# Kernel optimization log

Measured on AMD Instinct MI355X. Metric: run time of the kernel, lower is better.

The kernel has to match this reference:

```python
import jax, jax.numpy as jnp
import numpy as np

B, S, D = 4, 2048, 1024
O = 1024
E = 8
K = 2

def setup_inputs() -> dict:
    key = jax.random.key(0)
    k1, k2, k3, k4, k5 = jax.random.split(key, 5)
    scale = 1.0 / np.sqrt(D)
    x = jax.random.normal(k1, (B, S, D), dtype=jnp.float32)
    # expert linear layers stacked: weight [E, D, O], bias [E, O]
    We = jax.random.uniform(k2, (E, D, O), dtype=jnp.float32, minval=-scale, maxval=scale)
    be = jax.random.uniform(k3, (E, O), dtype=jnp.float32, minval=-scale, maxval=scale)
    # gate linear: weight [D, E], bias [E]
    Wg = jax.random.uniform(k4, (D, E), dtype=jnp.float32, minval=-scale, maxval=scale)
    bg = jax.random.uniform(k5, (E,), dtype=jnp.float32, minval=-scale, maxval=scale)
    return {"x": x, "We": We, "be": be, "Wg": Wg, "bg": bg}

def reference(x, We, be, Wg, bg):
    b, s, d = x.shape
    x_flat = x.reshape(-1, d)                                   # [N, D]
    gates = jax.nn.softmax(x_flat @ Wg + bg, axis=-1)           # [N, E]
    topk_gates, topk_idx = jax.lax.top_k(gates, K)              # [N, K]
    topk_gates = topk_gates / jnp.sum(topk_gates, axis=1, keepdims=True)
    # dense all-expert compute (faithful to original naive MoE)
    expert_out = jnp.einsum('nd,edo->neo', x_flat, We) + be     # [N, E, O]
    # gather top-k expert outputs per token
    selected = jnp.take_along_axis(expert_out, topk_idx[:, :, None], axis=1)  # [N, K, O]
    out = jnp.sum(selected * topk_gates[:, :, None], axis=1)    # [N, O]
    return out.reshape(b, s, -1)
```

## Files before the change

kernel.cpp:

```cpp
#include <hip/hip_runtime.h>

#define N_TOK 8192
#define DDIM 1024
#define ODIM 1024
#define NEXP 8

typedef __attribute__((ext_vector_type(8))) short bf16x8;
typedef __attribute__((ext_vector_type(4))) float f32x4;

__device__ __forceinline__ unsigned int f2bf(float f) {
    unsigned int u = __float_as_uint(f);
    return (u + 0x7fffu + ((u >> 16) & 1u)) >> 16;
}
__device__ __forceinline__ float bflo(unsigned int u) { return __uint_as_float(u << 16); }
__device__ __forceinline__ float bfhi(unsigned int u) { return __uint_as_float(u & 0xffff0000u); }

__device__ __forceinline__ void async_copy16(const unsigned short* g, unsigned short* l) {
    __builtin_amdgcn_global_load_lds(
        (const __attribute__((address_space(1))) unsigned int*)g,
        (__attribute__((address_space(3))) unsigned int*)l, 16, 0, 0);
}

__global__ __launch_bounds__(256) void gate_kernel(const float* __restrict__ x,
                                                   const float* __restrict__ Wg,
                                                   const float* __restrict__ bg,
                                                   int* __restrict__ ea, int* __restrict__ eb,
                                                   float* __restrict__ ga, float* __restrict__ gb,
                                                   unsigned short* __restrict__ xbf,
                                                   int* __restrict__ counts) {
    if (blockIdx.x == 0) counts[threadIdx.x] = 0;
    const int wave = threadIdx.x >> 6, lane = threadIdx.x & 63;
    const int t = blockIdx.x * 4 + wave;
    const float* xr = x + (size_t)t * DDIM;

    float4 v[4];
#pragma unroll
    for (int c = 0; c < 4; ++c) v[c] = *(const float4*)&xr[c * 256 + lane * 4];

    unsigned short* xo = xbf + (size_t)t * DDIM;
#pragma unroll
    for (int c = 0; c < 4; ++c) {
        uint2 w;
        w.x = f2bf(v[c].x) | (f2bf(v[c].y) << 16);
        w.y = f2bf(v[c].z) | (f2bf(v[c].w) << 16);
        *(uint2*)&xo[c * 256 + lane * 4] = w;
    }

    float acc[8] = {0, 0, 0, 0, 0, 0, 0, 0};
#pragma unroll
    for (int c = 0; c < 4; ++c) {
        const int dbase = c * 256 + lane * 4;
#pragma unroll
        for (int j = 0; j < 4; ++j) {
            float xv = ((const float*)&v[c])[j];
            const float4* w = (const float4*)(Wg + (size_t)(dbase + j) * 8);
            float4 w0 = w[0], w1 = w[1];
            acc[0] += xv * w0.x; acc[1] += xv * w0.y; acc[2] += xv * w0.z; acc[3] += xv * w0.w;
            acc[4] += xv * w1.x; acc[5] += xv * w1.y; acc[6] += xv * w1.z; acc[7] += xv * w1.w;
        }
    }
#pragma unroll
    for (int off = 32; off > 0; off >>= 1) {
#pragma unroll
        for (int j = 0; j < 8; ++j) acc[j] += __shfl_xor(acc[j], off, 64);
    }
    if (lane == 0) {
        float s[8];
#pragma unroll
        for (int e = 0; e < 8; ++e) s[e] = acc[e] + bg[e];
        int a = 0;
#pragma unroll
        for (int e = 1; e < 8; ++e) if (s[e] > s[a]) a = e;
        int b = (a == 0) ? 1 : 0;
#pragma unroll
        for (int e = 0; e < 8; ++e) if (e != a && e != b && s[e] > s[b]) b = e;
        float g0 = 1.0f / (1.0f + __expf(s[b] - s[a]));
        ea[t] = a; eb[t] = b; ga[t] = g0; gb[t] = 1.0f - g0;
    }
}

__global__ __launch_bounds__(256) void transpose_kernel(const float* __restrict__ We,
                                                        unsigned short* __restrict__ WeT) {
    __shared__ float tile[64][65];
    const int lin = blockIdx.x;
    const int e = lin >> 8, rem = lin & 255;
    const int d0 = (rem >> 4) * 64, o0 = (rem & 15) * 64;
    const int tid = threadIdx.x;
#pragma unroll
    for (int p = 0; p < 4; ++p) {
        int idx = p * 256 + tid;
        int row = idx >> 4, c = idx & 15;
        float4 v = *(const float4*)&We[(((size_t)e * 1024 + d0 + row) << 10) + o0 + (c << 2)];
        tile[row][c * 4 + 0] = v.x; tile[row][c * 4 + 1] = v.y;
        tile[row][c * 4 + 2] = v.z; tile[row][c * 4 + 3] = v.w;
    }
    __syncthreads();
#pragma unroll
    for (int p = 0; p < 2; ++p) {
        int idx = p * 256 + tid;
        int orow = idx >> 3, c8 = idx & 7;
        unsigned int u[8];
#pragma unroll
        for (int j = 0; j < 8; ++j) u[j] = f2bf(tile[c8 * 8 + j][orow]);
        uint4 q;
        q.x = u[0] | (u[1] << 16); q.y = u[2] | (u[3] << 16);
        q.z = u[4] | (u[5] << 16); q.w = u[6] | (u[7] << 16);
        *(uint4*)&WeT[(((size_t)e * 1024 + o0 + orow) << 10) + d0 + (c8 << 3)] = q;
    }
}

__global__ __launch_bounds__(64) void scatter_kernel(const int* __restrict__ ea,
                                                     const int* __restrict__ eb,
                                                     int* __restrict__ counts,
                                                     int* __restrict__ btok,
                                                     int* __restrict__ slotA,
                                                     int* __restrict__ slotB) {
    const int t = blockIdx.x * 64 + threadIdx.x;
    const int lane = threadIdx.x & 63;
#pragma unroll
    for (int pass = 0; pass < 2; ++pass) {
        const int e = (pass == 0) ? ea[t] : eb[t];
        int* slot = (pass == 0) ? slotA : slotB;
#pragma unroll
        for (int ex = 0; ex < NEXP; ++ex) {
            unsigned long long mask = __ballot(e == ex);
            if (mask) {
                int leader = __ffsll((long long)mask) - 1;
                int base = 0;
                if (lane == leader) base = atomicAdd(&counts[ex * 32], __popcll(mask));
                base = __shfl(base, leader, 64);
                if (e == ex) {
                    int pos = base + __popcll(mask & ((1ull << lane) - 1ull));
                    btok[ex * N_TOK + pos] = t;
                    slot[t] = ex * N_TOK + pos;
                }
            }
        }
    }
}

__global__ __launch_bounds__(256, 2) void moe_gemm(const unsigned short* __restrict__ xbf,
                                                   const unsigned short* __restrict__ WeT,
                                                   const float* __restrict__ be,
                                                   const int* __restrict__ counts,
                                                   const int* __restrict__ btok,
                                                   unsigned short* __restrict__ ybuf) {
    const int id = blockIdx.x;
    const int e = id & 7;
    const int n0 = ((id >> 3) & 7) * 128;
    const int r0 = (id >> 6) * 160;
    const int cnt = counts[e * 32];
    if (r0 >= cnt) return;

    __shared__ unsigned short smem[36864];
    __shared__ int s_tok[160];

    const int tid = threadIdx.x;
    if (tid < 160) {
        int r = r0 + tid;
        int rc = (r < cnt) ? r : (cnt - 1);
        s_tok[tid] = btok[e * N_TOK + rc];
    }
    const int w = tid >> 6, lane = tid & 63;
    __syncthreads();

    const int rsub = lane >> 3;
    const int colo = ((lane & 7) ^ rsub) * 8;
    unsigned int a_off[5], b_off[4];
#pragma unroll
    for (int p = 0; p < 5; ++p) {
        int row = p * 32 + w * 8 + rsub;
        a_off[p] = ((unsigned)s_tok[row] << 10) + colo;
    }
#pragma unroll
    for (int p = 0; p < 4; ++p) {
        int row = p * 32 + w * 8 + rsub;
        b_off[p] = ((unsigned)(e * 1024 + n0 + row) << 10) + colo;
    }
    const int ldsrow = w * 8;

    const int wm = (w >> 1) * 80, wn = (w & 1) * 64;
    const int quad = lane >> 4, rA = lane & 15;
    const int sw = rA & 7;
    const int cs0 = (quad ^ sw) * 8;
    const int cs1 = ((4 + quad) ^ sw) * 8;

    f32x4 acc[5][4];
#pragma unroll
    for (int mi = 0; mi < 5; ++mi)
#pragma unroll
        for (int ni = 0; ni < 4; ++ni) acc[mi][ni] = (f32x4){0.f, 0.f, 0.f, 0.f};

#pragma unroll
    for (int p = 0; p < 5; ++p)
        async_copy16(xbf + a_off[p], &smem[(p * 32 + ldsrow) * 64]);
#pragma unroll
    for (int p = 0; p < 4; ++p)
        async_copy16(WeT + b_off[p], &smem[20480 + (p * 32 + ldsrow) * 64]);
#pragma unroll
    for (int p = 0; p < 5; ++p)
        async_copy16(xbf + a_off[p] + 64, &smem[10240 + (p * 32 + ldsrow) * 64]);
#pragma unroll
    for (int p = 0; p < 4; ++p)
        async_copy16(WeT + b_off[p] + 64, &smem[28672 + (p * 32 + ldsrow) * 64]);
    asm volatile("s_waitcnt vmcnt(9)" ::: "memory");
    __builtin_amdgcn_s_barrier();
    __builtin_amdgcn_sched_barrier(0);

    bf16x8 a0[5], b0[4];
#pragma unroll
    for (int i = 0; i < 5; ++i) a0[i] = *(bf16x8*)&smem[(wm + i * 16 + rA) * 64 + cs0];
#pragma unroll
    for (int i = 0; i < 4; ++i) b0[i] = *(bf16x8*)&smem[20480 + (wn + i * 16 + rA) * 64 + cs0];

    for (int t = 0; t < 16; ++t) {
        const int cur = t & 1;
        unsigned short* sAc = smem + cur * 10240;
        unsigned short* sBc = smem + 20480 + cur * 8192;
        unsigned short* sAn = smem + (cur ^ 1) * 10240;
        unsigned short* sBn = smem + 20480 + (cur ^ 1) * 8192;

        bf16x8 a1[5], b1[4];
#pragma unroll
        for (int i = 0; i < 5; ++i) a1[i] = *(bf16x8*)&sAc[(wm + i * 16 + rA) * 64 + cs1];
#pragma unroll
        for (int i = 0; i < 4; ++i) b1[i] = *(bf16x8*)&sBc[(wn + i * 16 + rA) * 64 + cs1];
        __builtin_amdgcn_s_setprio(1);
#pragma unroll
        for (int mi = 0; mi < 5; ++mi)
#pragma unroll
            for (int ni = 0; ni < 4; ++ni)
                acc[mi][ni] = __builtin_amdgcn_mfma_f32_16x16x32_bf16(b0[ni], a0[mi], acc[mi][ni], 0, 0, 0);
        __builtin_amdgcn_s_setprio(0);

        asm volatile("s_waitcnt lgkmcnt(0)" ::: "memory");
        __builtin_amdgcn_sched_barrier(0);
        __builtin_amdgcn_s_barrier();
        __builtin_amdgcn_sched_barrier(0);

        if (t < 14) {
            const int ko = (t + 2) * 64;
#pragma unroll
            for (int p = 0; p < 5; ++p)
                async_copy16(xbf + a_off[p] + ko, &sAc[(p * 32 + ldsrow) * 64]);
#pragma unroll
            for (int p = 0; p < 4; ++p)
                async_copy16(WeT + b_off[p] + ko, &sBc[(p * 32 + ldsrow) * 64]);
        }
        if (t < 15) {
            if (t < 14) {
                asm volatile("s_waitcnt vmcnt(9)" ::: "memory");
            } else {
                asm volatile("s_waitcnt vmcnt(0)" ::: "memory");
            }
            __builtin_amdgcn_sched_barrier(0);
            __builtin_amdgcn_s_barrier();
            __builtin_amdgcn_sched_barrier(0);
#pragma unroll
            for (int i = 0; i < 5; ++i) a0[i] = *(bf16x8*)&sAn[(wm + i * 16 + rA) * 64 + cs0];
#pragma unroll
            for (int i = 0; i < 4; ++i) b0[i] = *(bf16x8*)&sBn[(wn + i * 16 + rA) * 64 + cs0];
        }

        __builtin_amdgcn_s_setprio(1);
#pragma unroll
        for (int mi = 0; mi < 5; ++mi)
#pragma unroll
            for (int ni = 0; ni < 4; ++ni)
                acc[mi][ni] = __builtin_amdgcn_mfma_f32_16x16x32_bf16(b1[ni], a1[mi], acc[mi][ni], 0, 0, 0);
        __builtin_amdgcn_s_setprio(0);
    }

    float4 bv[4];
#pragma unroll
    for (int ni = 0; ni < 4; ++ni)
        bv[ni] = *(const float4*)&be[(e << 10) + n0 + wn + ni * 16 + quad * 4];
#pragma unroll
    for (int mi = 0; mi < 5; ++mi) {
        const int lrow = wm + mi * 16 + rA;
        if (r0 + lrow < cnt) {
            unsigned short* yrow =
                ybuf + (((size_t)(e * N_TOK + r0 + lrow)) << 10) + n0 + wn + quad * 4;
#pragma unroll
            for (int ni = 0; ni < 4; ++ni) {
                uint2 pk;
                pk.x = f2bf(acc[mi][ni][0] + bv[ni].x) | (f2bf(acc[mi][ni][1] + bv[ni].y) << 16);
                pk.y = f2bf(acc[mi][ni][2] + bv[ni].z) | (f2bf(acc[mi][ni][3] + bv[ni].w) << 16);
                *(uint2*)&yrow[ni * 16] = pk;
            }
        }
    }
}

__global__ __launch_bounds__(256) void combine_kernel(const unsigned short* __restrict__ ybuf,
                                                      const int* __restrict__ slotA,
                                                      const int* __restrict__ slotB,
                                                      const float* __restrict__ ga,
                                                      const float* __restrict__ gb,
                                                      float* __restrict__ out) {
    const int wave = threadIdx.x >> 6, lane = threadIdx.x & 63;
    const int t = blockIdx.x * 4 + wave;
    const unsigned short* ra = ybuf + ((size_t)slotA[t] << 10);
    const unsigned short* rb = ybuf + ((size_t)slotB[t] << 10);
    const float a = ga[t], b = gb[t];
    float* orow = out + ((size_t)t << 10);
#pragma unroll
    for (int i = 0; i < 2; ++i) {
        int c = i * 512 + lane * 8;
        uint4 ua = *(const uint4*)&ra[c];
        uint4 ub = *(const uint4*)&rb[c];
        float4 o0, o1;
        o0.x = a * bflo(ua.x) + b * bflo(ub.x);
        o0.y = a * bfhi(ua.x) + b * bfhi(ub.x);
        o0.z = a * bflo(ua.y) + b * bflo(ub.y);
        o0.w = a * bfhi(ua.y) + b * bfhi(ub.y);
        o1.x = a * bflo(ua.z) + b * bflo(ub.z);
        o1.y = a * bfhi(ua.z) + b * bfhi(ub.z);
        o1.z = a * bflo(ua.w) + b * bflo(ub.w);
        o1.w = a * bfhi(ua.w) + b * bfhi(ub.w);
        *(float4*)&orow[c] = o0;
        *(float4*)&orow[c + 4] = o1;
    }
}

extern "C" void kernel_launch(void* const* d_in, const int* in_sizes, int n_in,
                              void* d_out, int out_size, void* d_ws, size_t ws_size,
                              hipStream_t stream) {
    const float* x  = (const float*)d_in[0];
    const float* We = (const float*)d_in[1];
    const float* be = (const float*)d_in[2];
    const float* Wg = (const float*)d_in[3];
    const float* bg = (const float*)d_in[4];
    float* out = (float*)d_out;

    char* ws = (char*)d_ws;
    size_t off = 0;
    int* counts = (int*)(ws + off); off += 8 * 32 * 4;
    int* btok   = (int*)(ws + off); off += NEXP * N_TOK * 4;
    int* slotA  = (int*)(ws + off); off += N_TOK * 4;
    int* slotB  = (int*)(ws + off); off += N_TOK * 4;
    int* ea = (int*)(ws + off); off += N_TOK * 4;
    int* eb = (int*)(ws + off); off += N_TOK * 4;
    float* ga = (float*)(ws + off); off += N_TOK * 4;
    float* gb = (float*)(ws + off); off += N_TOK * 4;
    unsigned short* WeT  = (unsigned short*)(ws + off); off += (size_t)NEXP * DDIM * ODIM * 2;
    unsigned short* xbf  = (unsigned short*)(ws + off); off += (size_t)N_TOK * DDIM * 2;
    unsigned short* ybuf = (unsigned short*)(ws + off); off += (size_t)NEXP * N_TOK * ODIM * 2;

    gate_kernel<<<dim3(2048), 256, 0, stream>>>(x, Wg, bg, ea, eb, ga, gb, xbf, counts);
    transpose_kernel<<<dim3(2048), 256, 0, stream>>>(We, WeT);
    scatter_kernel<<<dim3(N_TOK / 64), 64, 0, stream>>>(ea, eb, counts, btok, slotA, slotB);
    moe_gemm<<<dim3(64 * 8 * 8), 256, 0, stream>>>(xbf, WeT, be, counts, btok, ybuf);
    combine_kernel<<<dim3(N_TOK / 4), 256, 0, stream>>>(ybuf, slotA, slotB, ga, gb, out);
}
```

Measured before the change: 208.6 us.

## Fuse gate and transpose kernels, replace combine pass with atomic accumulation in GEMM epilogue

The gate and weight-transpose kernels merge into one prep kernel, which also zero-initialises the output. The separate combine kernel and the bf16 ybuf intermediate are removed. The GEMM epilogue now scales each row by its gate weight and float-atomically adds it directly into the output row of its token. This removes the write and re-read of the large expert-output buffer and one launch, at the cost of scalar float atomics and non-deterministic summation order.

After: 392.3 us. 88.0% more time.

```diff
diff --git a/kernel.cpp b/kernel.cpp
--- a/kernel.cpp
+++ b/kernel.cpp
@@ -12,8 +12,6 @@
     unsigned int u = __float_as_uint(f);
     return (u + 0x7fffu + ((u >> 16) & 1u)) >> 16;
 }
-__device__ __forceinline__ float bflo(unsigned int u) { return __uint_as_float(u << 16); }
-__device__ __forceinline__ float bfhi(unsigned int u) { return __uint_as_float(u & 0xffff0000u); }
 
 __device__ __forceinline__ void async_copy16(const unsigned short* g, unsigned short* l) {
     __builtin_amdgcn_global_load_lds(
@@ -21,106 +19,114 @@
         (__attribute__((address_space(3))) unsigned int*)l, 16, 0, 0);
 }
 
-__global__ __launch_bounds__(256) void gate_kernel(const float* __restrict__ x,
+__global__ __launch_bounds__(256) void prep_kernel(const float* __restrict__ x,
                                                    const float* __restrict__ Wg,
                                                    const float* __restrict__ bg,
+                                                   const float* __restrict__ We,
                                                    int* __restrict__ ea, int* __restrict__ eb,
                                                    float* __restrict__ ga, float* __restrict__ gb,
                                                    unsigned short* __restrict__ xbf,
-                                                   int* __restrict__ counts) {
-    if (blockIdx.x == 0) counts[threadIdx.x] = 0;
-    const int wave = threadIdx.x >> 6, lane = threadIdx.x & 63;
-    const int t = blockIdx.x * 4 + wave;
-    const float* xr = x + (size_t)t * DDIM;
-
-    float4 v[4];
-#pragma unroll
-    for (int c = 0; c < 4; ++c) v[c] = *(const float4*)&xr[c * 256 + lane * 4];
-
-    unsigned short* xo = xbf + (size_t)t * DDIM;
-#pragma unroll
-    for (int c = 0; c < 4; ++c) {
-        uint2 w;
-        w.x = f2bf(v[c].x) | (f2bf(v[c].y) << 16);
-        w.y = f2bf(v[c].z) | (f2bf(v[c].w) << 16);
-        *(uint2*)&xo[c * 256 + lane * 4] = w;
-    }
-
-    float acc[8] = {0, 0, 0, 0, 0, 0, 0, 0};
-#pragma unroll
-    for (int c = 0; c < 4; ++c) {
-        const int dbase = c * 256 + lane * 4;
-#pragma unroll
-        for (int j = 0; j < 4; ++j) {
-            float xv = ((const float*)&v[c])[j];
-            const float4* w = (const float4*)(Wg + (size_t)(dbase + j) * 8);
-            float4 w0 = w[0], w1 = w[1];
-            acc[0] += xv * w0.x; acc[1] += xv * w0.y; acc[2] += xv * w0.z; acc[3] += xv * w0.w;
-            acc[4] += xv * w1.x; acc[5] += xv * w1.y; acc[6] += xv * w1.z; acc[7] += xv * w1.w;
-        }
-    }
-#pragma unroll
-    for (int off = 32; off > 0; off >>= 1) {
-#pragma unroll
-        for (int j = 0; j < 8; ++j) acc[j] += __shfl_xor(acc[j], off, 64);
-    }
-    if (lane == 0) {
-        float s[8];
-#pragma unroll
-        for (int e = 0; e < 8; ++e) s[e] = acc[e] + bg[e];
-        int a = 0;
-#pragma unroll
-        for (int e = 1; e < 8; ++e) if (s[e] > s[a]) a = e;
-        int b = (a == 0) ? 1 : 0;
-#pragma unroll
-        for (int e = 0; e < 8; ++e) if (e != a && e != b && s[e] > s[b]) b = e;
-        float g0 = 1.0f / (1.0f + __expf(s[b] - s[a]));
-        ea[t] = a; eb[t] = b; ga[t] = g0; gb[t] = 1.0f - g0;
-    }
-}
-
-__global__ __launch_bounds__(256) void transpose_kernel(const float* __restrict__ We,
-                                                        unsigned short* __restrict__ WeT) {
+                                                   unsigned short* __restrict__ WeT,
+                                                   int* __restrict__ counts,
+                                                   float* __restrict__ out) {
     __shared__ float tile[64][65];
-    const int lin = blockIdx.x;
-    const int e = lin >> 8, rem = lin & 255;
-    const int d0 = (rem >> 4) * 64, o0 = (rem & 15) * 64;
-    const int tid = threadIdx.x;
-#pragma unroll
-    for (int p = 0; p < 4; ++p) {
-        int idx = p * 256 + tid;
-        int row = idx >> 4, c = idx & 15;
-        float4 v = *(const float4*)&We[(((size_t)e * 1024 + d0 + row) << 10) + o0 + (c << 2)];
-        tile[row][c * 4 + 0] = v.x; tile[row][c * 4 + 1] = v.y;
-        tile[row][c * 4 + 2] = v.z; tile[row][c * 4 + 3] = v.w;
-    }
-    __syncthreads();
-#pragma unroll
-    for (int p = 0; p < 2; ++p) {
-        int idx = p * 256 + tid;
-        int orow = idx >> 3, c8 = idx & 7;
-        unsigned int u[8];
-#pragma unroll
-        for (int j = 0; j < 8; ++j) u[j] = f2bf(tile[c8 * 8 + j][orow]);
-        uint4 q;
-        q.x = u[0] | (u[1] << 16); q.y = u[2] | (u[3] << 16);
-        q.z = u[4] | (u[5] << 16); q.w = u[6] | (u[7] << 16);
-        *(uint4*)&WeT[(((size_t)e * 1024 + o0 + orow) << 10) + d0 + (c8 << 3)] = q;
+    if (blockIdx.x < 2048) {
+        if (blockIdx.x == 0) counts[threadIdx.x] = 0;
+        const int wave = threadIdx.x >> 6, lane = threadIdx.x & 63;
+        const int t = blockIdx.x * 4 + wave;
+        const float* xr = x + (size_t)t * DDIM;
+
+        float* orow = out + ((size_t)t << 10);
+        const float4 z = {0.f, 0.f, 0.f, 0.f};
+#pragma unroll
+        for (int c = 0; c < 4; ++c) *(float4*)&orow[c * 256 + lane * 4] = z;
+
+        float4 v[4];
+#pragma unroll
+        for (int c = 0; c < 4; ++c) v[c] = *(const float4*)&xr[c * 256 + lane * 4];
+
+        unsigned short* xo = xbf + (size_t)t * DDIM;
+#pragma unroll
+        for (int c = 0; c < 4; ++c) {
+            uint2 w;
+            w.x = f2bf(v[c].x) | (f2bf(v[c].y) << 16);
+            w.y = f2bf(v[c].z) | (f2bf(v[c].w) << 16);
+            *(uint2*)&xo[c * 256 + lane * 4] = w;
+        }
+
+        float acc[8] = {0, 0, 0, 0, 0, 0, 0, 0};
+#pragma unroll
+        for (int c = 0; c < 4; ++c) {
+            const int dbase = c * 256 + lane * 4;
+#pragma unroll
+            for (int j = 0; j < 4; ++j) {
+                float xv = ((const float*)&v[c])[j];
+                const float4* w = (const float4*)(Wg + (size_t)(dbase + j) * 8);
+                float4 w0 = w[0], w1 = w[1];
+                acc[0] += xv * w0.x; acc[1] += xv * w0.y; acc[2] += xv * w0.z; acc[3] += xv * w0.w;
+                acc[4] += xv * w1.x; acc[5] += xv * w1.y; acc[6] += xv * w1.z; acc[7] += xv * w1.w;
+            }
+        }
+#pragma unroll
+        for (int off = 32; off > 0; off >>= 1) {
+#pragma unroll
+            for (int j = 0; j < 8; ++j) acc[j] += __shfl_xor(acc[j], off, 64);
+        }
+        if (lane == 0) {
+            float s[8];
+#pragma unroll
+            for (int e = 0; e < 8; ++e) s[e] = acc[e] + bg[e];
+            int a = 0;
+#pragma unroll
+            for (int e = 1; e < 8; ++e) if (s[e] > s[a]) a = e;
+            int b = (a == 0) ? 1 : 0;
+#pragma unroll
+            for (int e = 0; e < 8; ++e) if (e != a && e != b && s[e] > s[b]) b = e;
+            float g0 = 1.0f / (1.0f + __expf(s[b] - s[a]));
+            ea[t] = a; eb[t] = b; ga[t] = g0; gb[t] = 1.0f - g0;
+        }
+    } else {
+        const int lin = blockIdx.x - 2048;
+        const int e = lin >> 8, rem = lin & 255;
+        const int d0 = (rem >> 4) * 64, o0 = (rem & 15) * 64;
+        const int tid = threadIdx.x;
+#pragma unroll
+        for (int p = 0; p < 4; ++p) {
+            int idx = p * 256 + tid;
+            int row = idx >> 4, c = idx & 15;
+            float4 v = *(const float4*)&We[(((size_t)e * 1024 + d0 + row) << 10) + o0 + (c << 2)];
+            tile[row][c * 4 + 0] = v.x; tile[row][c * 4 + 1] = v.y;
+            tile[row][c * 4 + 2] = v.z; tile[row][c * 4 + 3] = v.w;
+        }
+        __syncthreads();
+#pragma unroll
+        for (int p = 0; p < 2; ++p) {
+            int idx = p * 256 + tid;
+            int orow = idx >> 3, c8 = idx & 7;
+            unsigned int u[8];
+#pragma unroll
+            for (int j = 0; j < 8; ++j) u[j] = f2bf(tile[c8 * 8 + j][orow]);
+            uint4 q;
+            q.x = u[0] | (u[1] << 16); q.y = u[2] | (u[3] << 16);
+            q.z = u[4] | (u[5] << 16); q.w = u[6] | (u[7] << 16);
+            *(uint4*)&WeT[(((size_t)e * 1024 + o0 + orow) << 10) + d0 + (c8 << 3)] = q;
+        }
     }
 }
 
 __global__ __launch_bounds__(64) void scatter_kernel(const int* __restrict__ ea,
                                                      const int* __restrict__ eb,
+                                                     const float* __restrict__ ga,
+                                                     const float* __restrict__ gb,
                                                      int* __restrict__ counts,
                                                      int* __restrict__ btok,
-                                                     int* __restrict__ slotA,
-                                                     int* __restrict__ slotB) {
+                                                     float* __restrict__ wtok) {
     const int t = blockIdx.x * 64 + threadIdx.x;
     const int lane = threadIdx.x & 63;
 #pragma unroll
     for (int pass = 0; pass < 2; ++pass) {
         const int e = (pass == 0) ? ea[t] : eb[t];
-        int* slot = (pass == 0) ? slotA : slotB;
+        const float wg = (pass == 0) ? ga[t] : gb[t];
 #pragma unroll
         for (int ex = 0; ex < NEXP; ++ex) {
             unsigned long long mask = __ballot(e == ex);
@@ -132,7 +138,7 @@
                 if (e == ex) {
                     int pos = base + __popcll(mask & ((1ull << lane) - 1ull));
                     btok[ex * N_TOK + pos] = t;
-                    slot[t] = ex * N_TOK + pos;
+                    wtok[ex * N_TOK + pos] = wg;
                 }
             }
         }
@@ -144,7 +150,8 @@
                                                    const float* __restrict__ be,
                                                    const int* __restrict__ counts,
                                                    const int* __restrict__ btok,
-                                                   unsigned short* __restrict__ ybuf) {
+                                                   const float* __restrict__ wtok,
+                                                   float* __restrict__ out) {
     const int id = blockIdx.x;
     const int e = id & 7;
     const int n0 = ((id >> 3) & 7) * 128;
@@ -279,47 +286,17 @@
     for (int mi = 0; mi < 5; ++mi) {
         const int lrow = wm + mi * 16 + rA;
         if (r0 + lrow < cnt) {
-            unsigned short* yrow =
-                ybuf + (((size_t)(e * N_TOK + r0 + lrow)) << 10) + n0 + wn + quad * 4;
+            const int tok = s_tok[lrow];
+            const float wgt = wtok[e * N_TOK + r0 + lrow];
+            float* orow = out + ((size_t)tok << 10) + n0 + wn + quad * 4;
 #pragma unroll
             for (int ni = 0; ni < 4; ++ni) {
-                uint2 pk;
-                pk.x = f2bf(acc[mi][ni][0] + bv[ni].x) | (f2bf(acc[mi][ni][1] + bv[ni].y) << 16);
-                pk.y = f2bf(acc[mi][ni][2] + bv[ni].z) | (f2bf(acc[mi][ni][3] + bv[ni].w) << 16);
-                *(uint2*)&yrow[ni * 16] = pk;
+                unsafeAtomicAdd(&orow[ni * 16 + 0], wgt * (acc[mi][ni][0] + bv[ni].x));
+                unsafeAtomicAdd(&orow[ni * 16 + 1], wgt * (acc[mi][ni][1] + bv[ni].y));
+                unsafeAtomicAdd(&orow[ni * 16 + 2], wgt * (acc[mi][ni][2] + bv[ni].z));
+                unsafeAtomicAdd(&orow[ni * 16 + 3], wgt * (acc[mi][ni][3] + bv[ni].w));
             }
         }
-    }
-}
-
-__global__ __launch_bounds__(256) void combine_kernel(const unsigned short* __restrict__ ybuf,
-                                                      const int* __restrict__ slotA,
-                                                      const int* __restrict__ slotB,
-                                                      const float* __restrict__ ga,
-                                                      const float* __restrict__ gb,
-                                                      float* __restrict__ out) {
-    const int wave = threadIdx.x >> 6, lane = threadIdx.x & 63;
-    const int t = blockIdx.x * 4 + wave;
-    const unsigned short* ra = ybuf + ((size_t)slotA[t] << 10);
-    const unsigned short* rb = ybuf + ((size_t)slotB[t] << 10);
-    const float a = ga[t], b = gb[t];
-    float* orow = out + ((size_t)t << 10);
-#pragma unroll
-    for (int i = 0; i < 2; ++i) {
-        int c = i * 512 + lane * 8;
-        uint4 ua = *(const uint4*)&ra[c];
-        uint4 ub = *(const uint4*)&rb[c];
-        float4 o0, o1;
-        o0.x = a * bflo(ua.x) + b * bflo(ub.x);
-        o0.y = a * bfhi(ua.x) + b * bfhi(ub.x);
-        o0.z = a * bflo(ua.y) + b * bflo(ub.y);
-        o0.w = a * bfhi(ua.y) + b * bfhi(ub.y);
-        o1.x = a * bflo(ua.z) + b * bflo(ub.z);
-        o1.y = a * bfhi(ua.z) + b * bfhi(ub.z);
-        o1.z = a * bflo(ua.w) + b * bflo(ub.w);
-        o1.w = a * bfhi(ua.w) + b * bfhi(ub.w);
-        *(float4*)&orow[c] = o0;
-        *(float4*)&orow[c + 4] = o1;
     }
 }
 
@@ -337,19 +314,15 @@
     size_t off = 0;
     int* counts = (int*)(ws + off); off += 8 * 32 * 4;
     int* btok   = (int*)(ws + off); off += NEXP * N_TOK * 4;
-    int* slotA  = (int*)(ws + off); off += N_TOK * 4;
-    int* slotB  = (int*)(ws + off); off += N_TOK * 4;
+    float* wtok = (float*)(ws + off); off += NEXP * N_TOK * 4;
     int* ea = (int*)(ws + off); off += N_TOK * 4;
     int* eb = (int*)(ws + off); off += N_TOK * 4;
     float* ga = (float*)(ws + off); off += N_TOK * 4;
     float* gb = (float*)(ws + off); off += N_TOK * 4;
     unsigned short* WeT  = (unsigned short*)(ws + off); off += (size_t)NEXP * DDIM * ODIM * 2;
     unsigned short* xbf  = (unsigned short*)(ws + off); off += (size_t)N_TOK * DDIM * 2;
-    unsigned short* ybuf = (unsigned short*)(ws + off); off += (size_t)NEXP * N_TOK * ODIM * 2;
-
-    gate_kernel<<<dim3(2048), 256, 0, stream>>>(x, Wg, bg, ea, eb, ga, gb, xbf, counts);
-    transpose_kernel<<<dim3(2048), 256, 0, stream>>>(We, WeT);
-    scatter_kernel<<<dim3(N_TOK / 64), 64, 0, stream>>>(ea, eb, counts, btok, slotA, slotB);
-    moe_gemm<<<dim3(64 * 8 * 8), 256, 0, stream>>>(xbf, WeT, be, counts, btok, ybuf);
-    combine_kernel<<<dim3(N_TOK / 4), 256, 0, stream>>>(ybuf, slotA, slotB, ga, gb, out);
-}
+
+    prep_kernel<<<dim3(4096), 256, 0, stream>>>(x, Wg, bg, We, ea, eb, ga, gb, xbf, WeT, counts, out);
+    scatter_kernel<<<dim3(N_TOK / 64), 64, 0, stream>>>(ea, eb, ga, gb, counts, btok, wtok);
+    moe_gemm<<<dim3(64 * 8 * 8), 256, 0, stream>>>(xbf, WeT, be, counts, btok, wtok, out);
+}
```
